# Optimization experiments

Hardware: AMD Instinct MI355X
Metric: run time of the kernel (lower is better)

## Reference

```python
import jax, jax.numpy as jnp
import numpy as np

NUM_HEADS = 12


def setup_inputs() -> dict:
    key = jax.random.key(0)
    ks = jax.random.split(key, 8)
    B, N, C = 1024, 196, 384
    hd = C // NUM_HEADS  # 32
    return {
        "x": jax.random.normal(ks[0], (B, N, C), jnp.float32),
        "qkv_w": jax.random.normal(ks[1], (3 * C, C), jnp.float32) * 0.02,
        "qkv_b": jax.random.normal(ks[2], (3 * C,), jnp.float32) * 0.02,
        "proj_w": jax.random.normal(ks[3], (C, C), jnp.float32) * 0.02,
        "proj_b": jax.random.normal(ks[4], (C,), jnp.float32) * 0.02,
        "dwc_w": jax.random.normal(ks[5], (hd, 1, 5, 5), jnp.float32) * 0.02,
        "dwc_b": jax.random.normal(ks[6], (hd,), jnp.float32) * 0.02,
        "pos_enc": jax.random.normal(ks[7], (1, N, C), jnp.float32) * 0.02,
    }


def reference(x, qkv_w, qkv_b, proj_w, proj_b, dwc_w, dwc_b, pos_enc):
    B, N, C = x.shape
    h = NUM_HEADS
    hd = C // h

    qkv = x @ qkv_w.T + qkv_b                      # [B, N, 3C]
    qkv = qkv.reshape(B, N, 3, C)
    q, k, v = qkv[:, :, 0], qkv[:, :, 1], qkv[:, :, 2]
    k = k + pos_enc[:, :N, :]
    q = jax.nn.relu(q)
    k = jax.nn.relu(k)

    def split_heads(t):  # [B, N, (h c)] -> [(B h), N, c]
        return t.reshape(B, N, h, hd).transpose(0, 2, 1, 3).reshape(B * h, N, hd)

    q, k, v = split_heads(q), split_heads(k), split_heads(v)
    i, j, c, d = q.shape[-2], k.shape[-2], k.shape[-1], v.shape[-1]

    z = 1.0 / (jnp.einsum('bic,bc->bi', q, k.sum(axis=1)) + 1e-6)  # [Bh, N]
    if i * j * (c + d) > c * d * (i + j):
        kv = jnp.einsum('bjc,bjd->bcd', k, v)                      # [Bh, c, d]
        out = jnp.einsum('bic,bcd,bi->bid', q, kv, z)
    else:
        qk = jnp.einsum('bic,bjc->bij', q, k)
        out = jnp.einsum('bij,bjd,bi->bid', qk, v, z)

    # depthwise conv residual on v: [(B h), N, c] -> NCHW window grid
    w = int(N ** 0.5)
    fm = v.reshape(B * h, w, w, hd).transpose(0, 3, 1, 2)          # [Bh, c, w, w]
    fm = jax.lax.conv_general_dilated(
        fm, dwc_w, window_strides=(1, 1), padding='SAME',
        feature_group_count=hd,
        dimension_numbers=('NCHW', 'OIHW', 'NCHW'))
    fm = fm + dwc_b[None, :, None, None]
    fm = fm.transpose(0, 2, 3, 1).reshape(B * h, N, hd)

    out = out + fm
    out = out.reshape(B, h, N, hd).transpose(0, 2, 1, 3).reshape(B, N, C)
    out = out @ proj_w.T + proj_b
    return out
```

## Files before the change

kernel.cpp:

```cpp
#include <hip/hip_runtime.h>
#include <hip/hip_fp16.h>
#include <cstdint>

#define DI __device__ __forceinline__

typedef __attribute__((ext_vector_type(8))) _Float16 hx8;
typedef __attribute__((ext_vector_type(16))) float f32x16;
typedef __attribute__((ext_vector_type(4))) float f4;
typedef unsigned short u16;
typedef unsigned int u32;
typedef unsigned long long u64;
typedef __attribute__((ext_vector_type(4))) u32 u32x4;

constexpr int NB = 1024;
constexpr int NN = 196;
constexpr int NC = 384;
constexpr int NH = 12;
constexpr int HD = 32;
constexpr int C3 = 3 * NC;
constexpr int PH = NN * HD;
constexpr int KP = 208;
constexpr int HP = 32 * KP;
constexpr int NHEADS = NB * NH;

constexpr size_t SZ_Q    = (size_t)NHEADS * PH * 2;
constexpr size_t SZ_TP   = (size_t)NHEADS * HP * 2;
constexpr size_t OFF_Q   = 0;
constexpr size_t OFF_K   = SZ_Q;
constexpr size_t OFF_V   = OFF_K + SZ_TP;
constexpr size_t OFF_WQF = OFF_V + SZ_TP;
constexpr size_t SZ_WQ   = (size_t)C3 * NC * 2;
constexpr size_t OFF_WPF = OFF_WQF + SZ_WQ;
constexpr size_t SZ_WP   = (size_t)NC * NC * 2;
constexpr size_t OFF_XF  = OFF_WPF + SZ_WP;

DI void gload_lds16(const void* g, void* l) {
  using GP = const void __attribute__((address_space(1)))*;
  using LP = void __attribute__((address_space(3)))*;
  __builtin_amdgcn_global_load_lds((GP)g, (LP)l, 16, 0, 0);
}

DI float h2f(u16 v)  { _Float16 h = __builtin_bit_cast(_Float16, v); return (float)h; }
DI u16   f2h(float f){ _Float16 h = (_Float16)f; return __builtin_bit_cast(u16, h); }

__global__ void split_weights(const float* __restrict__ qw, const float* __restrict__ pw,
                              u16* __restrict__ qf, u16* __restrict__ pf,
                              u16* ktg, u16* vtg)
{
  int i = blockIdx.x * 256 + threadIdx.x;
  if (i < C3 * NC) qf[i] = f2h(qw[i]);
  if (i < NC * NC) pf[i] = f2h(pw[i]);
  for (u32 t = (u32)i; t < 786432u; t += 442368u) {
    u32 head = t >> 6; int r = t & 63;
    u16* p = ((r & 32) ? vtg : ktg) + (size_t)head * HP + (size_t)(r & 31) * KP + 196;
    *(u64*)(p) = 0; *(u64*)(p + 4) = 0; *(u64*)(p + 8) = 0;
  }
}

__global__ void cvt_x_f16(const float* __restrict__ x, u16* __restrict__ xf)
{
  size_t i = ((size_t)blockIdx.x * 256 + threadIdx.x) * 8;
  f4 a = *(const f4*)(x + i);
  f4 b = *(const f4*)(x + i + 4);
  u16 o[8];
  o[0]=f2h(a[0]); o[1]=f2h(a[1]); o[2]=f2h(a[2]); o[3]=f2h(a[3]);
  o[4]=f2h(b[0]); o[5]=f2h(b[1]); o[6]=f2h(b[2]); o[7]=f2h(b[3]);
  u32x4 pk;
#pragma unroll
  for (int j = 0; j < 4; ++j) pk[j] = (u32)o[2*j] | ((u32)o[2*j+1] << 16);
  *(u32x4*)(xf + i) = pk;
}

__global__ __launch_bounds__(256, 4) void qkv_gemm_f16(
    const u16* __restrict__ xf, const u16* __restrict__ wf,
    const float* __restrict__ bias, const float* __restrict__ pos,
    u16* __restrict__ qo, u16* __restrict__ ko, u16* __restrict__ vo)
{
  __shared__ __align__(16) char lds[2][16384];
  const int tid  = threadIdx.x;
  const int lane = tid & 63, wv = tid >> 6;
  const int L  = ((int)blockIdx.x & 7) * 1764 + ((int)blockIdx.x >> 3);
  const int rt = L / 9, ct = L - rt * 9;
  const int m0 = rt * 128, t0 = ct * 128;

  const u16* spA[2];
  const u16* spB[2];
#pragma unroll
  for (int j = 0; j < 2; ++j) {
    int g = j * 256 + tid;
    int row = g >> 2, slot = g & 3;
    int c = slot ^ (row & 3);
    spA[j] = xf + (size_t)(m0 + row) * NC + c * 8;
    spB[j] = wf + (size_t)(t0 + row) * NC + c * 8;
  }

  auto stage = [&](char* buf) {
#pragma unroll
    for (int j = 0; j < 2; ++j) {
      gload_lds16(spA[j], buf + (j * 256 + tid) * 16);
      spA[j] += 32;
      gload_lds16(spB[j], buf + 8192 + (j * 256 + tid) * 16);
      spB[j] += 32;
    }
  };

  const int wm = (wv & 1) * 64, wn = (wv >> 1) * 64;
  const int l15 = lane & 15, l4 = lane >> 4;
  const int sl = l4 ^ (l15 & 3);
  int aoff[4], boff[4];
#pragma unroll
  for (int i = 0; i < 4; ++i) {
    aoff[i] = (wm + i * 16 + l15) * 64 + sl * 16;
    boff[i] = 8192 + (wn + i * 16 + l15) * 64 + sl * 16;
  }

  f4 acc[4][4];
  const f4 fz = {0.f, 0.f, 0.f, 0.f};
#pragma unroll
  for (int i = 0; i < 4; ++i)
#pragma unroll
    for (int j = 0; j < 4; ++j) acc[i][j] = fz;

  stage(lds[0]);
  for (int kt = 0; kt < 12; ++kt) {
    __syncthreads();
    if (kt < 11) stage(lds[(kt + 1) & 1]);
    char* buf = lds[kt & 1];
    hx8 af[4], bf4[4];
#pragma unroll
    for (int i = 0; i < 4; ++i) {
      af[i]  = *(const hx8*)(buf + aoff[i]);
      bf4[i] = *(const hx8*)(buf + boff[i]);
    }
#pragma unroll
    for (int mi = 0; mi < 4; ++mi)
#pragma unroll
      for (int ni = 0; ni < 4; ++ni)
        acc[mi][ni] = __builtin_amdgcn_mfma_f32_16x16x32_f16(af[mi], bf4[ni], acc[mi][ni], 0, 0, 0);
  }

  const int s = ct / 3, cb = (ct - s * 3) * 128;
  float biasv[4];
#pragma unroll
  for (int ni = 0; ni < 4; ++ni) biasv[ni] = bias[t0 + wn + ni * 16 + l15];

  if (s == 0) {
#pragma unroll
    for (int mi = 0; mi < 4; ++mi) {
#pragma unroll
      for (int rr = 0; rr < 4; ++rr) {
        int m = m0 + wm + mi * 16 + l4 * 4 + rr;
        int b = m / 196, n = m - b * 196;
#pragma unroll
        for (int ni = 0; ni < 4; ++ni) {
          int c = cb + wn + ni * 16 + l15;
          float val = acc[mi][ni][rr] + biasv[ni];
          qo[((size_t)b * 12 + (c >> 5)) * PH + (size_t)n * 32 + (c & 31)] = f2h(fmaxf(val, 0.f));
        }
      }
    }
  } else {
    u16* outp = (s == 1) ? ko : vo;
    u16* tb = (u16*)&lds[0][0];
    __syncthreads();
#pragma unroll
    for (int p = 0; p < 2; ++p) {
      if (wm == p * 64) {
#pragma unroll
        for (int mi = 0; mi < 4; ++mi) {
#pragma unroll
          for (int ni = 0; ni < 4; ++ni) {
            int cl = wn + ni * 16 + l15;
            u64 w = 0;
#pragma unroll
            for (int rr = 0; rr < 4; ++rr) {
              int m = m0 + wm + mi * 16 + l4 * 4 + rr;
              int b = m / 196, n = m - b * 196;
              float val = acc[mi][ni][rr] + biasv[ni];
              if (s == 1) val = fmaxf(val + pos[n * 384 + cb + cl], 0.f);
              w |= (u64)f2h(val) << (rr * 16);
            }
            *(u64*)(tb + (size_t)cl * 72 + (mi * 16 + l4 * 4)) = w;
          }
        }
      }
      __syncthreads();
      {
        int r = tid >> 1, h = tid & 1;
        int cgl = cb + r, head = cgl >> 5, cc = cgl & 31;
        const u16* src = tb + (size_t)r * 72 + h * 32;
#pragma unroll
        for (int e = 0; e < 4; ++e) {
          u32x4 dd = *(const u32x4*)(src + e * 8);
          int mg = m0 + p * 64 + h * 32 + e * 8;
          int b = mg / 196, n = mg - b * 196;
          if (n <= 188) {
            u16* gp = outp + ((size_t)b * 12 + head) * HP + (size_t)cc * KP + n;
            *(u64*)gp       = ((const u64*)&dd)[0];
            *(u64*)(gp + 4) = ((const u64*)&dd)[1];
          } else {
            const u16* du = (const u16*)&dd;
#pragma unroll
            for (int ee = 0; ee < 8; ++ee) {
              int m2 = mg + ee, b2 = m2 / 196, n2 = m2 - b2 * 196;
              outp[((size_t)b2 * 12 + head) * HP + (size_t)cc * KP + n2] = du[ee];
            }
          }
        }
      }
      __syncthreads();
    }
  }
}

__global__ __launch_bounds__(256, 4) void attn_conv(
    const u16* __restrict__ q, const u16* kt, const u16* __restrict__ vt,
    u16* y, const float* __restrict__ dwc_w, const float* __restrict__ dwc_b)
{
  __shared__ __align__(16) char smem[30096];
  u16*   sKT = (u16*)smem;
  u16*   sVT = (u16*)(smem + 13312);
  u16*   sKV = (u16*)(smem + 26624);
  float* sZ  = (float*)(smem + 29184);
  float* sKS = (float*)(smem + 29968);

  const int tid  = threadIdx.x;
  const int lane = tid & 63, wv = tid >> 6;
  const int r31 = lane & 31, hi = lane >> 5;
  const size_t bh = blockIdx.x;
  const u16* qh = q  + bh * PH;
  const u16* kh = kt + bh * HP;
  const u16* vh = vt + bh * HP;
  u16*       yh = y  + bh * HP;

  for (int i = tid; i < 832; i += 256) gload_lds16(kh + i * 8, smem + i * 16);
  for (int i = tid; i < 832; i += 256) gload_lds16(vh + i * 8, smem + 13312 + i * 16);
  __syncthreads();

  if (wv == 0) {
    f32x16 kacc = {0,0,0,0,0,0,0,0,0,0,0,0,0,0,0,0};
#pragma unroll
    for (int kk = 0; kk < 13; ++kk) {
      hx8 a = *(const hx8*)(sKT + r31 * KP + kk * 16 + hi * 8);
      hx8 b = *(const hx8*)(sVT + r31 * KP + kk * 16 + hi * 8);
      kacc = __builtin_amdgcn_mfma_f32_32x32x16_f16(a, b, kacc, 0, 0, 0);
    }
#pragma unroll
    for (int r = 0; r < 16; ++r) {
      int cc = (r & 3) + 8 * (r >> 2) + 4 * hi;
      sKV[r31 * 40 + cc] = f2h(kacc[r]);
    }
  }

  {
    int c = tid >> 3, ns = tid & 7;
    float s = 0.f;
#pragma unroll
    for (int i = 0; i < 26; ++i) s += h2f(sKT[c * KP + ns * 26 + i]);
#pragma unroll
    for (int off = 1; off <= 4; off <<= 1) s += __shfl_xor(s, off);
    if (ns == 0) sKS[c] = s;
  }
  __syncthreads();

  if (tid < 196) {
    float pz = 0.f;
#pragma unroll
    for (int g = 0; g < 4; ++g) {
      u32x4 qw = *(const u32x4*)(qh + (size_t)tid * 32 + g * 8);
#pragma unroll
      for (int j = 0; j < 4; ++j) {
        pz += h2f((u16)(qw[j] & 0xffffu)) * sKS[g * 8 + 2 * j]
            + h2f((u16)(qw[j] >> 16))     * sKS[g * 8 + 2 * j + 1];
      }
    }
    sZ[tid] = 1.f / (pz + 1e-6f);
  }

  u16* sFM = sKT;
  auto conv_unit = [&](int u) {
    int d = u & 31, py = u >> 5;
    float fm[14];
    float bv = dwc_b[d];
#pragma unroll
    for (int px = 0; px < 14; ++px) fm[px] = bv;
#pragma unroll
    for (int ky = 0; ky < 5; ++ky) {
      int yy = py + ky - 2;
      if (yy < 0 || yy >= 14) continue;
      float w[5];
#pragma unroll
      for (int t = 0; t < 5; ++t) w[t] = dwc_w[d * 25 + ky * 5 + t];
      float r[14];
      const u32* vrow = (const u32*)(sVT + d * KP + yy * 14);
#pragma unroll
      for (int x2 = 0; x2 < 7; ++x2) {
        u32 pr = vrow[x2];
        r[2 * x2]     = h2f((u16)(pr & 0xffffu));
        r[2 * x2 + 1] = h2f((u16)(pr >> 16));
      }
#pragma unroll
      for (int px = 0; px < 14; ++px) {
#pragma unroll
        for (int kx = 0; kx < 5; ++kx) {
          int xx = px + kx - 2;
          if (xx < 0 || xx > 13) continue;
          fm[px] += w[kx] * r[xx];
        }
      }
    }
#pragma unroll
    for (int px = 0; px < 14; ++px)
      sFM[d * KP + py * 14 + px] = f2h(fm[px]);
  };
  conv_unit(tid);
  if (tid >= 64) conv_unit(tid + 192);
  __syncthreads();

#pragma unroll
  for (int rep = 0; rep < 2; ++rep) {
    int T = wv + rep * 4;
    if (T >= 7) break;
    const u16* qrow = qh + (size_t)(T * 32 + r31) * 32;
    f32x16 acc = {0,0,0,0,0,0,0,0,0,0,0,0,0,0,0,0};
#pragma unroll
    for (int s = 0; s < 2; ++s) {
      hx8 a = *(const hx8*)(qrow + hi * 8 + s * 16);
      hx8 b = *(const hx8*)(sKV + r31 * 40 + hi * 8 + s * 16);
      acc = __builtin_amdgcn_mfma_f32_32x32x16_f16(a, b, acc, 0, 0, 0);
    }
#pragma unroll
    for (int r = 0; r < 16; ++r) {
      int row = (r & 3) + 8 * (r >> 2) + 4 * hi;
      int n = T * 32 + row;
      if (n < 196) {
        float val = acc[r] * sZ[n] + h2f(sFM[r31 * KP + n]);
        yh[n * 32 + r31] = f2h(val);
      }
    }
  }
}

__global__ __launch_bounds__(256, 4) void proj_gemm_f16(
    const u16* __restrict__ yf, const u16* __restrict__ wf,
    const float* __restrict__ bias, float* __restrict__ out)
{
  __shared__ __align__(16) char lds[2][16384];
  const int tid  = threadIdx.x;
  const int lane = tid & 63, wv = tid >> 6;
  const int L  = ((int)blockIdx.x & 7) * 588 + ((int)blockIdx.x >> 3);
  const int rt = L / 3, ct = L - rt * 3;
  const int m0 = rt * 128, t0 = ct * 128;

  const u16* spA[2];
  const u16* spB[2];
#pragma unroll
  for (int j = 0; j < 2; ++j) {
    int g = j * 256 + tid;
    int row = g >> 2, slot = g & 3;
    int c = slot ^ (row & 3);
    int m = m0 + row;
    int b = m / 196, n = m - b * 196;
    spA[j] = yf + (size_t)b * (12 * HP) + (size_t)n * 32 + c * 8;
    spB[j] = wf + (size_t)(t0 + row) * NC + c * 8;
  }

  auto stage = [&](char* buf) {
#pragma unroll
    for (int j = 0; j < 2; ++j) {
      gload_lds16(spA[j], buf + (j * 256 + tid) * 16);
      spA[j] += HP;
      gload_lds16(spB[j], buf + 8192 + (j * 256 + tid) * 16);
      spB[j] += 32;
    }
  };

  const int wm = (wv & 1) * 64, wn = (wv >> 1) * 64;
  const int l15 = lane & 15, l4 = lane >> 4;
  const int sl = l4 ^ (l15 & 3);
  int aoff[4], boff[4];
#pragma unroll
  for (int i = 0; i < 4; ++i) {
    aoff[i] = (wm + i * 16 + l15) * 64 + sl * 16;
    boff[i] = 8192 + (wn + i * 16 + l15) * 64 + sl * 16;
  }

  f4 acc[4][4];
  const f4 fz = {0.f, 0.f, 0.f, 0.f};
#pragma unroll
  for (int i = 0; i < 4; ++i)
#pragma unroll
    for (int j = 0; j < 4; ++j) acc[i][j] = fz;

  stage(lds[0]);
  for (int kt = 0; kt < 12; ++kt) {
    __syncthreads();
    if (kt < 11) stage(lds[(kt + 1) & 1]);
    char* buf = lds[kt & 1];
    hx8 af[4], bf4[4];
#pragma unroll
    for (int i = 0; i < 4; ++i) {
      af[i]  = *(const hx8*)(buf + aoff[i]);
      bf4[i] = *(const hx8*)(buf + boff[i]);
    }
#pragma unroll
    for (int mi = 0; mi < 4; ++mi)
#pragma unroll
      for (int ni = 0; ni < 4; ++ni)
        acc[mi][ni] = __builtin_amdgcn_mfma_f32_16x16x32_f16(af[mi], bf4[ni], acc[mi][ni], 0, 0, 0);
  }

  float biasv[4];
#pragma unroll
  for (int ni = 0; ni < 4; ++ni) biasv[ni] = bias[t0 + wn + ni * 16 + l15];
#pragma unroll
  for (int mi = 0; mi < 4; ++mi) {
#pragma unroll
    for (int rr = 0; rr < 4; ++rr) {
      int m = m0 + wm + mi * 16 + l4 * 4 + rr;
      size_t ob = (size_t)m * 384 + t0 + wn;
#pragma unroll
      for (int ni = 0; ni < 4; ++ni)
        out[ob + ni * 16 + l15] = acc[mi][ni][rr] + biasv[ni];
    }
  }
}

extern "C" void kernel_launch(void* const* d_in, const int* in_sizes, int n_in,
                              void* d_out, int out_size, void* d_ws, size_t ws_size,
                              hipStream_t stream)
{
  const float* x      = (const float*)d_in[0];
  const float* qkv_w  = (const float*)d_in[1];
  const float* qkv_b  = (const float*)d_in[2];
  const float* proj_w = (const float*)d_in[3];
  const float* proj_b = (const float*)d_in[4];
  const float* dwc_w  = (const float*)d_in[5];
  const float* dwc_b  = (const float*)d_in[6];
  const float* pos    = (const float*)d_in[7];
  float* out = (float*)d_out;
  char* ws = (char*)d_ws;

  u16* qb  = (u16*)(ws + OFF_Q);
  u16* kb  = (u16*)(ws + OFF_K);
  u16* vb  = (u16*)(ws + OFF_V);
  u16* wqf = (u16*)(ws + OFF_WQF);
  u16* wpf = (u16*)(ws + OFF_WPF);
  u16* xf  = (u16*)(ws + OFF_XF);
  u16* yb  = (u16*)(ws + OFF_K);

  split_weights<<<1728, 256, 0, stream>>>(qkv_w, proj_w, wqf, wpf, kb, vb);
  cvt_x_f16<<<37632, 256, 0, stream>>>(x, xf);
  qkv_gemm_f16<<<14112, 256, 0, stream>>>(xf, wqf, qkv_b, pos, qb, kb, vb);
  attn_conv<<<12288, 256, 0, stream>>>(qb, kb, vb, yb, dwc_w, dwc_b);
  proj_gemm_f16<<<4704, 256, 0, stream>>>(yb, wpf, proj_b, out);
}
```

Before: 885.8 us.

## Enlarge QKV and projection GEMM tiles to 256x128 with 512-thread blocks

Both fp16 GEMMs now use 256-row by 128-column output tiles, computed by 8 waves in 512-thread blocks instead of 128x128 tiles with 4 waves. Each weight tile staged in LDS is shared by twice as many output rows, which cuts global and LDS traffic for B per unit of output. Grid sizes and the block-swizzle constants are halved, and the transposed K/V epilogue runs four 64-row passes instead of two. The cost is more LDS per block (48KB), fewer resident blocks per CU, and a longer serialized epilogue.

```diff
diff --git a/kernel.cpp b/kernel.cpp
--- a/kernel.cpp
+++ b/kernel.cpp
@@ -71,47 +71,51 @@
   *(u32x4*)(xf + i) = pk;
 }
 
-__global__ __launch_bounds__(256, 4) void qkv_gemm_f16(
+__global__ __launch_bounds__(512, 6) void qkv_gemm_f16(
     const u16* __restrict__ xf, const u16* __restrict__ wf,
     const float* __restrict__ bias, const float* __restrict__ pos,
     u16* __restrict__ qo, u16* __restrict__ ko, u16* __restrict__ vo)
 {
-  __shared__ __align__(16) char lds[2][16384];
+  __shared__ __align__(16) char lds[2][24576];
   const int tid  = threadIdx.x;
   const int lane = tid & 63, wv = tid >> 6;
-  const int L  = ((int)blockIdx.x & 7) * 1764 + ((int)blockIdx.x >> 3);
+  const int L  = ((int)blockIdx.x & 7) * 882 + ((int)blockIdx.x >> 3);
   const int rt = L / 9, ct = L - rt * 9;
-  const int m0 = rt * 128, t0 = ct * 128;
+  const int m0 = rt * 256, t0 = ct * 128;
 
   const u16* spA[2];
-  const u16* spB[2];
+  const u16* spB;
 #pragma unroll
   for (int j = 0; j < 2; ++j) {
-    int g = j * 256 + tid;
+    int g = j * 512 + tid;
     int row = g >> 2, slot = g & 3;
     int c = slot ^ (row & 3);
     spA[j] = xf + (size_t)(m0 + row) * NC + c * 8;
-    spB[j] = wf + (size_t)(t0 + row) * NC + c * 8;
+  }
+  {
+    int row = tid >> 2, slot = tid & 3;
+    int c = slot ^ (row & 3);
+    spB = wf + (size_t)(t0 + row) * NC + c * 8;
   }
 
   auto stage = [&](char* buf) {
 #pragma unroll
     for (int j = 0; j < 2; ++j) {
-      gload_lds16(spA[j], buf + (j * 256 + tid) * 16);
+      gload_lds16(spA[j], buf + (j * 512 + tid) * 16);
       spA[j] += 32;
-      gload_lds16(spB[j], buf + 8192 + (j * 256 + tid) * 16);
-      spB[j] += 32;
-    }
+    }
+    gload_lds16(spB, buf + 16384 + tid * 16);
+    spB += 32;
   };
 
-  const int wm = (wv & 1) * 64, wn = (wv >> 1) * 64;
+  const int wm = (wv >> 1) * 64, wn = (wv & 1) * 64;
   const int l15 = lane & 15, l4 = lane >> 4;
   const int sl = l4 ^ (l15 & 3);
   int aoff[4], boff[4];
 #pragma unroll
   for (int i = 0; i < 4; ++i) {
     aoff[i] = (wm + i * 16 + l15) * 64 + sl * 16;
-    boff[i] = 8192 + (wn + i * 16 + l15) * 64 + sl * 16;
+    boff[i] = 16384 + (wn + i * 16 + l15) * 64 + sl * 16;
   }
 
   f4 acc[4][4];
@@ -164,7 +168,7 @@
     u16* tb = (u16*)&lds[0][0];
     __syncthreads();
 #pragma unroll
-    for (int p = 0; p < 2; ++p) {
+    for (int p = 0; p < 4; ++p) {
       if (wm == p * 64) {
 #pragma unroll
         for (int mi = 0; mi < 4; ++mi) {
@@ -186,13 +190,13 @@
       }
       __syncthreads();
       {
-        int r = tid >> 1, h = tid & 1;
+        int r = tid >> 2, h = tid & 3;
         int cgl = cb + r, head = cgl >> 5, cc = cgl & 31;
-        const u16* src = tb + (size_t)r * 72 + h * 32;
-#pragma unroll
-        for (int e = 0; e < 4; ++e) {
-          u32x4 dd = *(const u32x4*)(src + e * 8);
-          int mg = m0 + p * 64 + h * 32 + e * 8;
+#pragma unroll
+        for (int e = 0; e < 2; ++e) {
+          const u16* src = tb + (size_t)r * 72 + h * 16 + e * 8;
+          u32x4 dd = *(const u32x4*)src;
+          int mg = m0 + p * 64 + h * 16 + e * 8;
           int b = mg / 196, n = mg - b * 196;
           if (n <= 188) {
             u16* gp = outp + ((size_t)b * 12 + head) * HP + (size_t)cc * KP + n;
@@ -341,48 +345,52 @@
   }
 }
 
-__global__ __launch_bounds__(256, 4) void proj_gemm_f16(
+__global__ __launch_bounds__(512, 6) void proj_gemm_f16(
     const u16* __restrict__ yf, const u16* __restrict__ wf,
     const float* __restrict__ bias, float* __restrict__ out)
 {
-  __shared__ __align__(16) char lds[2][16384];
+  __shared__ __align__(16) char lds[2][24576];
   const int tid  = threadIdx.x;
   const int lane = tid & 63, wv = tid >> 6;
-  const int L  = ((int)blockIdx.x & 7) * 588 + ((int)blockIdx.x >> 3);
+  const int L  = ((int)blockIdx.x & 7) * 294 + ((int)blockIdx.x >> 3);
   const int rt = L / 3, ct = L - rt * 3;
-  const int m0 = rt * 128, t0 = ct * 128;
+  const int m0 = rt * 256, t0 = ct * 128;
 
   const u16* spA[2];
-  const u16* spB[2];
+  const u16* spB;
 #pragma unroll
   for (int j = 0; j < 2; ++j) {
-    int g = j * 256 + tid;
+    int g = j * 512 + tid;
     int row = g >> 2, slot = g & 3;
     int c = slot ^ (row & 3);
     int m = m0 + row;
     int b = m / 196, n = m - b * 196;
     spA[j] = yf + (size_t)b * (12 * HP) + (size_t)n * 32 + c * 8;
-    spB[j] = wf + (size_t)(t0 + row) * NC + c * 8;
+  }
+  {
+    int row = tid >> 2, slot = tid & 3;
+    int c = slot ^ (row & 3);
+    spB = wf + (size_t)(t0 + row) * NC + c * 8;
   }
 
   auto stage = [&](char* buf) {
 #pragma unroll
     for (int j = 0; j < 2; ++j) {
-      gload_lds16(spA[j], buf + (j * 256 + tid) * 16);
+      gload_lds16(spA[j], buf + (j * 512 + tid) * 16);
       spA[j] += HP;
-      gload_lds16(spB[j], buf + 8192 + (j * 256 + tid) * 16);
-      spB[j] += 32;
-    }
+    }
+    gload_lds16(spB, buf + 16384 + tid * 16);
+    spB += 32;
   };
 
-  const int wm = (wv & 1) * 64, wn = (wv >> 1) * 64;
+  const int wm = (wv >> 1) * 64, wn = (wv & 1) * 64;
   const int l15 = lane & 15, l4 = lane >> 4;
   const int sl = l4 ^ (l15 & 3);
   int aoff[4], boff[4];
 #pragma unroll
   for (int i = 0; i < 4; ++i) {
     aoff[i] = (wm + i * 16 + l15) * 64 + sl * 16;
-    boff[i] = 8192 + (wn + i * 16 + l15) * 64 + sl * 16;
+    boff[i] = 16384 + (wn + i * 16 + l15) * 64 + sl * 16;
   }
 
   f4 acc[4][4];
@@ -451,7 +459,7 @@
 
   split_weights<<<1728, 256, 0, stream>>>(qkv_w, proj_w, wqf, wpf, kb, vb);
   cvt_x_f16<<<37632, 256, 0, stream>>>(x, xf);
-  qkv_gemm_f16<<<14112, 256, 0, stream>>>(xf, wqf, qkv_b, pos, qb, kb, vb);
+  qkv_gemm_f16<<<7056, 512, 0, stream>>>(xf, wqf, qkv_b, pos, qb, kb, vb);
   attn_conv<<<12288, 256, 0, stream>>>(qb, kb, vb, yb, dwc_w, dwc_b);
-  proj_gemm_f16<<<4704, 256, 0, stream>>>(yb, wpf, proj_b, out);
-}
+  proj_gemm_f16<<<2352, 512, 0, stream>>>(yb, wpf, proj_b, out);
+}
```

Result: slower. 1.794 ms (+102.5%).

## Widen QKV GEMM tile to 128x384 with A fragments loaded directly from global

Applied to the files above, without the earlier changes.

The QKV GEMM now uses 512-thread blocks, each computing a 128-row by 384-column tile that covers a full q, k or v section. This cuts the block count to a third and reuses each weight tile across more rows. The A operand (activations) is no longer staged through LDS. Each wave loads its fragments straight from global memory, prefetched one k-step ahead, while only the weights go through double-buffered LDS. This raises registers per thread (24 accumulators) and relies on the cache for A reuse across the four column waves. The transpose epilogue is reworked for the wider tile.

```diff
diff --git a/kernel.cpp b/kernel.cpp
--- a/kernel.cpp
+++ b/kernel.cpp
@@ -71,78 +71,83 @@
   *(u32x4*)(xf + i) = pk;
 }
 
-__global__ __launch_bounds__(256, 4) void qkv_gemm_f16(
+__global__ __launch_bounds__(512, 2) void qkv_gemm_f16(
     const u16* __restrict__ xf, const u16* __restrict__ wf,
     const float* __restrict__ bias, const float* __restrict__ pos,
     u16* __restrict__ qo, u16* __restrict__ ko, u16* __restrict__ vo)
 {
-  __shared__ __align__(16) char lds[2][16384];
+  __shared__ __align__(16) char lds[2][24576];
   const int tid  = threadIdx.x;
   const int lane = tid & 63, wv = tid >> 6;
-  const int L  = ((int)blockIdx.x & 7) * 1764 + ((int)blockIdx.x >> 3);
-  const int rt = L / 9, ct = L - rt * 9;
-  const int m0 = rt * 128, t0 = ct * 128;
-
-  const u16* spA[2];
-  const u16* spB[2];
-#pragma unroll
-  for (int j = 0; j < 2; ++j) {
-    int g = j * 256 + tid;
+  const int L  = ((int)blockIdx.x & 7) * 588 + ((int)blockIdx.x >> 3);
+  const int rt = L / 3, s = L - rt * 3;
+  const int m0 = rt * 128;
+  const u16* wfs = wf + (size_t)s * 384 * NC;
+
+  const u16* spB[3];
+#pragma unroll
+  for (int j = 0; j < 3; ++j) {
+    int g = j * 512 + tid;
     int row = g >> 2, slot = g & 3;
     int c = slot ^ (row & 3);
-    spA[j] = xf + (size_t)(m0 + row) * NC + c * 8;
-    spB[j] = wf + (size_t)(t0 + row) * NC + c * 8;
-  }
-
+    spB[j] = wfs + (size_t)row * NC + c * 8;
+  }
   auto stage = [&](char* buf) {
 #pragma unroll
-    for (int j = 0; j < 2; ++j) {
-      gload_lds16(spA[j], buf + (j * 256 + tid) * 16);
-      spA[j] += 32;
-      gload_lds16(spB[j], buf + 8192 + (j * 256 + tid) * 16);
+    for (int j = 0; j < 3; ++j) {
+      gload_lds16(spB[j], buf + (j * 512 + tid) * 16);
       spB[j] += 32;
     }
   };
 
-  const int wm = (wv & 1) * 64, wn = (wv >> 1) * 64;
+  const int wm = (wv >> 2) * 64, wn = (wv & 3) * 96;
   const int l15 = lane & 15, l4 = lane >> 4;
   const int sl = l4 ^ (l15 & 3);
-  int aoff[4], boff[4];
-#pragma unroll
-  for (int i = 0; i < 4; ++i) {
-    aoff[i] = (wm + i * 16 + l15) * 64 + sl * 16;
-    boff[i] = 8192 + (wn + i * 16 + l15) * 64 + sl * 16;
-  }
-
-  f4 acc[4][4];
+  const u16* ap[4];
+#pragma unroll
+  for (int i = 0; i < 4; ++i)
+    ap[i] = xf + (size_t)(m0 + wm + i * 16 + l15) * NC + l4 * 8;
+  int boff[6];
+#pragma unroll
+  for (int i = 0; i < 6; ++i)
+    boff[i] = (wn + i * 16 + l15) * 64 + sl * 16;
+
+  f4 acc[4][6];
   const f4 fz = {0.f, 0.f, 0.f, 0.f};
 #pragma unroll
   for (int i = 0; i < 4; ++i)
 #pragma unroll
-    for (int j = 0; j < 4; ++j) acc[i][j] = fz;
+    for (int j = 0; j < 6; ++j) acc[i][j] = fz;
 
   stage(lds[0]);
+  hx8 afn[4];
+#pragma unroll
+  for (int i = 0; i < 4; ++i) { afn[i] = *(const hx8*)ap[i]; ap[i] += 32; }
+
   for (int kt = 0; kt < 12; ++kt) {
     __syncthreads();
     if (kt < 11) stage(lds[(kt + 1) & 1]);
     char* buf = lds[kt & 1];
-    hx8 af[4], bf4[4];
-#pragma unroll
-    for (int i = 0; i < 4; ++i) {
-      af[i]  = *(const hx8*)(buf + aoff[i]);
-      bf4[i] = *(const hx8*)(buf + boff[i]);
-    }
+    hx8 af[4];
+#pragma unroll
+    for (int i = 0; i < 4; ++i) af[i] = afn[i];
+    if (kt < 11) {
+#pragma unroll
+      for (int i = 0; i < 4; ++i) { afn[i] = *(const hx8*)ap[i]; ap[i] += 32; }
+    }
+    hx8 bf[6];
+#pragma unroll
+    for (int i = 0; i < 6; ++i) bf[i] = *(const hx8*)(buf + boff[i]);
 #pragma unroll
     for (int mi = 0; mi < 4; ++mi)
 #pragma unroll
-      for (int ni = 0; ni < 4; ++ni)
-        acc[mi][ni] = __builtin_amdgcn_mfma_f32_16x16x32_f16(af[mi], bf4[ni], acc[mi][ni], 0, 0, 0);
-  }
-
-  const int s = ct / 3, cb = (ct - s * 3) * 128;
-  float biasv[4];
-#pragma unroll
-  for (int ni = 0; ni < 4; ++ni) biasv[ni] = bias[t0 + wn + ni * 16 + l15];
+      for (int ni = 0; ni < 6; ++ni)
+        acc[mi][ni] = __builtin_amdgcn_mfma_f32_16x16x32_f16(af[mi], bf[ni], acc[mi][ni], 0, 0, 0);
+  }
+
+  float biasv[6];
+#pragma unroll
+  for (int ni = 0; ni < 6; ++ni) biasv[ni] = bias[s * 384 + wn + ni * 16 + l15];
 
   if (s == 0) {
 #pragma unroll
@@ -152,8 +157,8 @@
         int m = m0 + wm + mi * 16 + l4 * 4 + rr;
         int b = m / 196, n = m - b * 196;
 #pragma unroll
-        for (int ni = 0; ni < 4; ++ni) {
-          int c = cb + wn + ni * 16 + l15;
+        for (int ni = 0; ni < 6; ++ni) {
+          int c = wn + ni * 16 + l15;
           float val = acc[mi][ni][rr] + biasv[ni];
           qo[((size_t)b * 12 + (c >> 5)) * PH + (size_t)n * 32 + (c & 31)] = f2h(fmaxf(val, 0.f));
         }
@@ -163,36 +168,36 @@
     u16* outp = (s == 1) ? ko : vo;
     u16* tb = (u16*)&lds[0][0];
     __syncthreads();
-#pragma unroll
-    for (int p = 0; p < 2; ++p) {
-      if (wm == p * 64) {
+    for (int p = 0; p < 4; ++p) {
+      if ((wv & 3) == p) {
 #pragma unroll
         for (int mi = 0; mi < 4; ++mi) {
 #pragma unroll
-          for (int ni = 0; ni < 4; ++ni) {
-            int cl = wn + ni * 16 + l15;
+          for (int ni = 0; ni < 6; ++ni) {
+            int cl = ni * 16 + l15;
+            int ml = wm + mi * 16 + l4 * 4;
             u64 w = 0;
 #pragma unroll
             for (int rr = 0; rr < 4; ++rr) {
-              int m = m0 + wm + mi * 16 + l4 * 4 + rr;
+              int m = m0 + ml + rr;
               int b = m / 196, n = m - b * 196;
               float val = acc[mi][ni][rr] + biasv[ni];
-              if (s == 1) val = fmaxf(val + pos[n * 384 + cb + cl], 0.f);
+              if (s == 1) val = fmaxf(val + pos[n * 384 + wn + ni * 16 + l15], 0.f);
               w |= (u64)f2h(val) << (rr * 16);
             }
-            *(u64*)(tb + (size_t)cl * 72 + (mi * 16 + l4 * 4)) = w;
+            *(u64*)(tb + (size_t)cl * 136 + ml) = w;
           }
         }
       }
       __syncthreads();
-      {
-        int r = tid >> 1, h = tid & 1;
-        int cgl = cb + r, head = cgl >> 5, cc = cgl & 31;
-        const u16* src = tb + (size_t)r * 72 + h * 32;
+      if (tid < 384) {
+        int r = tid >> 2, qd = tid & 3;
+        int c = p * 96 + r, head = c >> 5, cc = c & 31;
 #pragma unroll
         for (int e = 0; e < 4; ++e) {
-          u32x4 dd = *(const u32x4*)(src + e * 8);
-          int mg = m0 + p * 64 + h * 32 + e * 8;
+          const u16* src = tb + (size_t)r * 136 + qd * 32 + e * 8;
+          u32x4 dd = *(const u32x4*)src;
+          int mg = m0 + qd * 32 + e * 8;
           int b = mg / 196, n = mg - b * 196;
           if (n <= 188) {
             u16* gp = outp + ((size_t)b * 12 + head) * HP + (size_t)cc * KP + n;
@@ -451,7 +456,7 @@
 
   split_weights<<<1728, 256, 0, stream>>>(qkv_w, proj_w, wqf, wpf, kb, vb);
   cvt_x_f16<<<37632, 256, 0, stream>>>(x, xf);
-  qkv_gemm_f16<<<14112, 256, 0, stream>>>(xf, wqf, qkv_b, pos, qb, kb, vb);
+  qkv_gemm_f16<<<4704, 512, 0, stream>>>(xf, wqf, qkv_b, pos, qb, kb, vb);
   attn_conv<<<12288, 256, 0, stream>>>(qb, kb, vb, yb, dwc_w, dwc_b);
   proj_gemm_f16<<<4704, 256, 0, stream>>>(yb, wpf, proj_b, out);
 }
```

After: 1.272 ms. 1.44x slower.
